# Kernel tuning notes

Hardware: AMD Instinct MI355X
Metric: run time of the kernel (lower is better)

Reference implementation:

```python
import jax, jax.numpy as jnp
import numpy as np

G = 128          # grid_size
C = 256          # feature_dim
H = 4            # n_heads
D = C // H       # d_head
LN_EPS = 1e-5


def setup_inputs() -> dict:
    key = jax.random.key(0)
    ks = jax.random.split(key, 8)
    B, N = 2, 100000
    inp = {
        "GS_feats": jax.random.normal(ks[0], (B, N, C), jnp.float32),
        "scene_bounds": jnp.array([-1.0, 1.0, -1.0, 1.0, -1.0, 1.0], jnp.float32),
        "q_xy": jax.random.normal(ks[1], (C, G, G), jnp.float32),
        "q_xz": jax.random.normal(ks[2], (C, G, G), jnp.float32),
        "q_yz": jax.random.normal(ks[3], (C, G, G), jnp.float32),
        "to_k_w": jax.random.normal(ks[4], (C, C), jnp.float32) * (C ** -0.5),
        "to_k_b": jnp.zeros((C,), jnp.float32),
        "to_v_w": jax.random.normal(ks[5], (C, C), jnp.float32) * (C ** -0.5),
        "to_v_b": jnp.zeros((C,), jnp.float32),
        "ln_g": jnp.ones((C,), jnp.float32),
        "ln_b": jnp.zeros((C,), jnp.float32),
    }
    return inp


def _layernorm(x, g, b):
    mu = jnp.mean(x, axis=-1, keepdims=True)
    var = jnp.mean(jnp.square(x - mu), axis=-1, keepdims=True)
    return (x - mu) * jax.lax.rsqrt(var + LN_EPS) * g + b


def _forward(GS_feats, scene_bounds, q_xy, q_xz, q_yz,
             to_k_w, to_k_b, to_v_w, to_v_b, ln_g, ln_b):
    lo = scene_bounds[0::2]  # (xmin, ymin, zmin)
    hi = scene_bounds[1::2]  # (xmax, ymax, zmax)
    G2 = G * G

    def per_batch(pts):  # pts: [N, C]
        # normalize xyz to [-1, 1] per scene bounds, keep remaining channels
        coords = 2.0 * (pts[:, :3] - lo) / (hi - lo) - 1.0          # [N, 3]
        feats = jnp.concatenate([coords, pts[:, 3:]], axis=-1)      # [N, C]
        fn = _layernorm(feats, ln_g, ln_b)
        k = (fn @ to_k_w.T + to_k_b).reshape(-1, H, D)              # [N, H, D]
        v = (fn @ to_v_w.T + to_v_b).reshape(-1, H, D)              # [N, H, D]

        planes = []
        for q_param, (a0, a1) in ((q_xy, (0, 1)), (q_xz, (0, 2)), (q_yz, (1, 2))):
            pc = coords[:, (a0, a1)]                                 # [N, 2]
            gc = ((pc * 0.5 + 0.5) * (G - 1)).astype(jnp.int32)
            gc = jnp.clip(gc, 0, G - 1)
            idx = gc[:, 0] * G + gc[:, 1]                            # cell per point
            # per-cell learned queries: [G2, H, D]
            qc = q_param.reshape(C, G2).T.reshape(G2, H, D)
            s = jnp.sum(k * qc[idx], axis=-1)                        # [N, H] scores
            # segment softmax over points within each cell
            smax = jax.ops.segment_max(s, idx, num_segments=G2)      # [G2, H]
            smax = jnp.where(jnp.isfinite(smax), smax, 0.0)          # empty cells
            e = jnp.exp(s - smax[idx])                               # [N, H]
            den = jax.ops.segment_sum(e, idx, num_segments=G2)       # [G2, H]
            w = e / jnp.maximum(den[idx], 1e-30)                     # [N, H]
            out = jax.ops.segment_sum(w[:, :, None] * v, idx, num_segments=G2)  # [G2,H,D]
            # original does .view(C, G, G) on the [G2, C] tensor (raw reshape)
            planes.append(out.reshape(G2, C).reshape(C, G, G))
        return jnp.stack(planes)                                     # [3, C, G, G]

    return jax.vmap(per_batch)(GS_feats)                             # [B, 3, C, G, G]


def reference(GS_feats, scene_bounds, q_xy, q_xz, q_yz,
              to_k_w, to_k_b, to_v_w, to_v_b, ln_g, ln_b):
    return _forward(GS_feats, scene_bounds, q_xy, q_xz, q_yz,
                    to_k_w, to_k_b, to_v_w, to_v_b, ln_g, ln_b)
```

## Files before the change

kernel.cpp:

```cpp
#include <hip/hip_runtime.h>
#include <hip/hip_bf16.h>

#define GG 128
#define G2 (GG*GG)
#define CC 256
#define HH 4
#define NPTS 100000
#define NB 2
#define LN_EPS 1e-5f
#define CHUNK 256

typedef __attribute__((ext_vector_type(8))) short short8v;
typedef __attribute__((ext_vector_type(4))) float float4v;

__device__ __forceinline__ unsigned short bfround(float x){
    unsigned u = __float_as_uint(x);
    return (unsigned short)((u + 0x7FFFu + ((u >> 16) & 1u)) >> 16);
}
__device__ __forceinline__ float bfval(unsigned short h){
    return __uint_as_float(((unsigned)h) << 16);
}

__global__ __launch_bounds__(256) void prep_b2_kernel(
    const float* __restrict__ Wk, const float* __restrict__ Wv,
    const float* __restrict__ kb, const float* __restrict__ vb,
    unsigned short* __restrict__ B2, float* __restrict__ bias_comb)
{
    int n = blockIdx.x;
    int t = threadIdx.x;
    const float* src = (n < 256) ? (Wk + (size_t)n*CC) : (Wv + (size_t)(n-256)*CC);
    float w = src[t];
    unsigned short h = bfround(w);
    unsigned short l = bfround(w - bfval(h));
    unsigned short* row = B2 + (size_t)n*768;
    row[t] = h;
    row[256 + t] = l;
    row[512 + t] = h;
    if (t == 0) bias_comb[n] = (n < 256) ? kb[n] : vb[n-256];
}

__global__ __launch_bounds__(256) void transpose_q_kernel(
    const float* __restrict__ qxy, const float* __restrict__ qxz,
    const float* __restrict__ qyz, float* __restrict__ qT)
{
    int blk = blockIdx.x;
    int plane = blk >> 10;
    int rem = blk & 1023;
    int cell0 = (rem >> 2) << 6;
    int c0 = (rem & 3) << 6;
    const float* q = plane == 0 ? qxy : (plane == 1 ? qxz : qyz);
    __shared__ float tile[64][65];
    int tx = threadIdx.x & 63;
    int ty = threadIdx.x >> 6;
    #pragma unroll
    for (int i = ty; i < 64; i += 4)
        tile[i][tx] = q[(size_t)(c0 + i)*G2 + cell0 + tx];
    __syncthreads();
    #pragma unroll
    for (int i = ty; i < 64; i += 4)
        qT[((size_t)plane*G2 + cell0 + i)*CC + c0 + tx] = tile[tx][i];
}

__global__ __launch_bounds__(256, 4) void point_kernel(
    const float* __restrict__ feats, const float* __restrict__ bounds,
    const unsigned short* __restrict__ B2, const float* __restrict__ bias_comb,
    const float* __restrict__ lng, const float* __restrict__ lnb,
    const float* __restrict__ qT,
    unsigned short* __restrict__ Vout, float* __restrict__ s_out,
    int* __restrict__ cnt)
{
    __shared__ __align__(16) char lraw[34176];
    unsigned short* Ahi = (unsigned short*)lraw;
    unsigned short* Alo = (unsigned short*)(lraw + 16896);
    float* K_f = (float*)lraw;
    float* coords_lds = (float*)(lraw + 33792);

    int t = threadIdx.x;
    int lane = t & 63;
    int w = t >> 6;
    long long g0 = (long long)blockIdx.x * 32;
    int b  = (int)(g0 / NPTS);
    int pt0 = (int)(g0 % NPTS);

    float xr[8][4];
    #pragma unroll
    for (int r = 0; r < 8; r++){
        int p = w*8 + r;
        const float* f = feats + ((size_t)b*NPTS + pt0 + p)*CC;
        xr[r][0] = f[lane];
        xr[r][1] = f[lane + 64];
        xr[r][2] = f[lane + 128];
        xr[r][3] = f[lane + 192];
    }

    float lg0 = lng[lane], lg1 = lng[lane+64], lg2 = lng[lane+128], lg3 = lng[lane+192];
    float lb0 = lnb[lane], lb1 = lnb[lane+64], lb2 = lnb[lane+128], lb3 = lnb[lane+192];
    #pragma unroll
    for (int r = 0; r < 8; r++){
        int p = w*8 + r;
        float x0 = xr[r][0], x1 = xr[r][1], x2 = xr[r][2], x3 = xr[r][3];
        if (lane < 3){
            float l0 = bounds[2*lane], h0 = bounds[2*lane+1];
            float tnum = __fmul_rn(2.0f, __fsub_rn(x0, l0));
            float cv = __fsub_rn(__fdiv_rn(tnum, __fsub_rn(h0, l0)), 1.0f);
            x0 = cv;
            coords_lds[p*3 + lane] = cv;
        }
        float s1 = x0 + x1 + x2 + x3;
        float s2 = x0*x0 + x1*x1 + x2*x2 + x3*x3;
        #pragma unroll
        for (int off = 32; off; off >>= 1){
            s1 += __shfl_xor(s1, off);
            s2 += __shfl_xor(s2, off);
        }
        float mu = s1 * (1.0f/CC);
        float var = s2 * (1.0f/CC) - mu*mu;
        float rs = rsqrtf(var + LN_EPS);

        float f0 = (x0 - mu)*rs*lg0 + lb0;
        float f1 = (x1 - mu)*rs*lg1 + lb1;
        float f2 = (x2 - mu)*rs*lg2 + lb2;
        float f3 = (x3 - mu)*rs*lg3 + lb3;
        unsigned short h0 = bfround(f0), h1 = bfround(f1);
        unsigned short h2 = bfround(f2), h3 = bfround(f3);
        Ahi[p*264 + lane      ] = h0;  Alo[p*264 + lane      ] = bfround(f0 - bfval(h0));
        Ahi[p*264 + lane +  64] = h1;  Alo[p*264 + lane +  64] = bfround(f1 - bfval(h1));
        Ahi[p*264 + lane + 128] = h2;  Alo[p*264 + lane + 128] = bfround(f2 - bfval(h2));
        Ahi[p*264 + lane + 192] = h3;  Alo[p*264 + lane + 192] = bfround(f3 - bfval(h3));
    }
    __syncthreads();

    {
        int apt = lane & 15;
        int krow = (lane >> 4) * 8;
        int n0 = w * 128;
        int bcol = n0 + (lane & 15);
        float4v acc0[8], acc1[8];
        #pragma unroll
        for (int ni = 0; ni < 8; ni++){
            float bz = bias_comb[n0 + ni*16 + (lane & 15)];
            acc0[ni][0]=bz; acc0[ni][1]=bz; acc0[ni][2]=bz; acc0[ni][3]=bz;
            acc1[ni][0]=bz; acc1[ni][1]=bz; acc1[ni][2]=bz; acc1[ni][3]=bz;
        }
        #pragma unroll 2
        for (int ks = 0; ks < 24; ks++){
            int term = ks >> 3;
            int kk = (ks & 7)*32 + krow;
            int kglob = term*256 + kk;
            const unsigned short* Abase = (term < 2) ? Ahi : Alo;
            short8v a0 = *reinterpret_cast<const short8v*>(Abase + apt*264 + kk);
            short8v a1 = *reinterpret_cast<const short8v*>(Abase + (16+apt)*264 + kk);
            #pragma unroll
            for (int ni = 0; ni < 8; ni++){
                short8v bf = *reinterpret_cast<const short8v*>(
                    B2 + (size_t)(bcol + ni*16)*768 + kglob);
                acc0[ni] = __builtin_amdgcn_mfma_f32_16x16x32_bf16(a0, bf, acc0[ni], 0, 0, 0);
                acc1[ni] = __builtin_amdgcn_mfma_f32_16x16x32_bf16(a1, bf, acc1[ni], 0, 0, 0);
            }
        }
        __syncthreads();
        if (w < 2){
            #pragma unroll
            for (int ni = 0; ni < 8; ni++){
                int ch = n0 + ni*16 + (lane & 15);
                #pragma unroll
                for (int r4 = 0; r4 < 4; r4++){
                    int pt = (lane >> 4)*4 + r4;
                    K_f[pt*260 + ch]        = acc0[ni][r4];
                    K_f[(16 + pt)*260 + ch] = acc1[ni][r4];
                }
            }
        } else {
            #pragma unroll
            for (int ni = 0; ni < 8; ni++){
                int ch = (n0 - 256) + ni*16 + (lane & 15);
                #pragma unroll
                for (int r4 = 0; r4 < 4; r4++){
                    int pt = (lane >> 4)*4 + r4;
                    Vout[((size_t)b*NPTS + pt0 + pt)*CC + ch]        = bfround(acc0[ni][r4]);
                    Vout[((size_t)b*NPTS + pt0 + 16 + pt)*CC + ch]   = bfround(acc1[ni][r4]);
                }
            }
        }
    }
    __syncthreads();

    {
        int grp = lane >> 3;
        int g   = lane & 7;
        int h   = g >> 1;
        int p   = w*8 + grp;
        int pt  = pt0 + p;
        float cx = coords_lds[p*3], cy = coords_lds[p*3+1], cz = coords_lds[p*3+2];

        float4 k4[8];
        {
            const float4* Krow = reinterpret_cast<const float4*>(&K_f[p*260 + g*32]);
            #pragma unroll
            for (int j = 0; j < 8; j++) k4[j] = Krow[j];
        }
        int cells[3];
        #pragma unroll
        for (int pl = 0; pl < 3; pl++){
            float a = (pl == 2) ? cy : cx;
            float bb = (pl == 0) ? cy : cz;
            float ua = __fmul_rn(__fadd_rn(__fmul_rn(a, 0.5f), 0.5f), (float)(GG-1));
            float ub = __fmul_rn(__fadd_rn(__fmul_rn(bb,0.5f), 0.5f), (float)(GG-1));
            int gx = (int)ua; gx = gx < 0 ? 0 : (gx > GG-1 ? GG-1 : gx);
            int gy = (int)ub; gy = gy < 0 ? 0 : (gy > GG-1 ? GG-1 : gy);
            cells[pl] = gx*GG + gy;
        }
        #pragma unroll
        for (int pl = 0; pl < 3; pl++){
            int cell = cells[pl];
            const float4* qrow = reinterpret_cast<const float4*>(
                qT + ((size_t)pl*G2 + cell)*CC + g*32);
            float a0 = 0.f, a1 = 0.f, a2 = 0.f, a3 = 0.f;
            #pragma unroll
            for (int j = 0; j < 8; j++){
                float4 q4 = qrow[j];
                a0 = fmaf(k4[j].x, q4.x, a0);
                a1 = fmaf(k4[j].y, q4.y, a1);
                a2 = fmaf(k4[j].z, q4.z, a2);
                a3 = fmaf(k4[j].w, q4.w, a3);
            }
            float sh = (a0 + a1) + (a2 + a3);
            sh += __shfl_xor(sh, 1);
            if ((lane & 1) == 0){
                int bp = b*3 + pl;
                s_out[((size_t)bp*NPTS + pt)*HH + h] = sh;
                if (g == 0) atomicAdd(&cnt[(size_t)bp*G2 + cell], 1);
            }
        }
    }
}

__global__ __launch_bounds__(1024) void scan_kernel(
    const int* __restrict__ cnt, int* __restrict__ startm,
    int* __restrict__ worklist, int* __restrict__ nwork)
{
    __shared__ int sums[1024];
    __shared__ int sumc[1024];
    const int PER = (NB*3*G2) / 1024;
    int t = threadIdx.x;
    int base = t * PER;
    int s = 0, sc = 0;
    for (int i = 0; i < PER; i++){
        int c = cnt[base + i];
        s += c;
        sc += (c + CHUNK-1) >> 8;
    }
    sums[t] = s; sumc[t] = sc;
    __syncthreads();
    for (int off = 1; off < 1024; off <<= 1){
        int v  = (t >= off) ? sums[t - off] : 0;
        int vc = (t >= off) ? sumc[t - off] : 0;
        __syncthreads();
        sums[t] += v; sumc[t] += vc;
        __syncthreads();
    }
    int excl  = (t == 0) ? 0 : sums[t - 1];
    int exclc = (t == 0) ? 0 : sumc[t - 1];
    for (int i = 0; i < PER; i++){
        int c = cnt[base + i];
        startm[base + i] = excl;
        excl += c;
        int nch = (c + CHUNK-1) >> 8;
        for (int ci = 0; ci < nch; ci++)
            worklist[exclc++] = ((base + i) << 8) | ci;
    }
    if (t == 1023) nwork[0] = exclc;
}

__global__ __launch_bounds__(256) void fill_kernel(
    const float* __restrict__ feats, const float* __restrict__ bounds,
    int* __restrict__ startm, int* __restrict__ plist)
{
    int g = blockIdx.x * 256 + threadIdx.x;
    if (g >= NB*NPTS) return;
    int b = g / NPTS, pt = g % NPTS;
    const float* f = feats + (size_t)g*CC;
    float c3[3];
    #pragma unroll
    for (int a = 0; a < 3; a++){
        float lo = bounds[2*a], hi = bounds[2*a+1];
        float tn = __fmul_rn(2.0f, __fsub_rn(f[a], lo));
        c3[a] = __fsub_rn(__fdiv_rn(tn, __fsub_rn(hi, lo)), 1.0f);
    }
    #pragma unroll
    for (int pl = 0; pl < 3; pl++){
        float a = (pl == 2) ? c3[1] : c3[0];
        float bb = (pl == 0) ? c3[1] : c3[2];
        float ua = __fmul_rn(__fadd_rn(__fmul_rn(a, 0.5f), 0.5f), (float)(GG-1));
        float ub = __fmul_rn(__fadd_rn(__fmul_rn(bb,0.5f), 0.5f), (float)(GG-1));
        int gx = (int)ua; gx = gx < 0 ? 0 : (gx > GG-1 ? GG-1 : gx);
        int gy = (int)ub; gy = gy < 0 ? 0 : (gy > GG-1 ? GG-1 : gy);
        int cellg = (b*3 + pl)*G2 + gx*GG + gy;
        int pos = atomicAdd(&startm[cellg], 1);
        plist[pos] = pt;
    }
}

__global__ __launch_bounds__(256) void gather_kernel(
    const int* __restrict__ plist, const int* __restrict__ startm,
    const int* __restrict__ cnt, const float* __restrict__ s_in,
    const unsigned short* __restrict__ V, const int* __restrict__ worklist,
    const int* __restrict__ nwork, float* __restrict__ out,
    float* __restrict__ den_tmp)
{
    int lane = threadIdx.x & 63;
    int wi = blockIdx.x * 4 + (threadIdx.x >> 6);
    if (wi >= nwork[0]) return;
    int item = worklist[wi];
    int cellg = item >> 8;
    int ci = item & 255;
    int bp = cellg >> 14;
    int b = bp / 3;
    int h = lane >> 4;

    int end = startm[cellg];
    int n = cnt[cellg];
    int begin = end - n;

    const unsigned short* Vb = V + (size_t)b*NPTS*CC;
    const float* sb = s_in + (size_t)bp*NPTS*HH;

    float m0 = -INFINITY, m1 = -INFINITY, m2 = -INFINITY, m3 = -INFINITY;
    for (int chunk = begin; chunk < end; chunk += 64){
        int i = chunk + lane;
        if (i < end){
            int p = plist[i];
            float4 sv = *reinterpret_cast<const float4*>(sb + (size_t)p*HH);
            m0 = fmaxf(m0, sv.x); m1 = fmaxf(m1, sv.y);
            m2 = fmaxf(m2, sv.z); m3 = fmaxf(m3, sv.w);
        }
    }
    #pragma unroll
    for (int off = 32; off; off >>= 1){
        m0 = fmaxf(m0, __shfl_xor(m0, off));
        m1 = fmaxf(m1, __shfl_xor(m1, off));
        m2 = fmaxf(m2, __shfl_xor(m2, off));
        m3 = fmaxf(m3, __shfl_xor(m3, off));
    }
    float smh = (h == 0) ? m0 : (h == 1) ? m1 : (h == 2) ? m2 : m3;

    int cb = begin + ci*CHUNK;
    int ce = min(cb + CHUNK, end);
    float ax = 0.f, ay = 0.f, az = 0.f, aw = 0.f, den = 0.f;
    for (int chunk = cb; chunk < ce; chunk += 64){
        int m = min(64, ce - chunk);
        int pid = (lane < m) ? plist[chunk + lane] : 0;
        int j = 0;
        for (; j + 4 <= m; j += 4){
            int p0 = __shfl(pid, j  ), p1 = __shfl(pid, j+1);
            int p2 = __shfl(pid, j+2), p3 = __shfl(pid, j+3);
            float e0 = expf(sb[(size_t)p0*HH + h] - smh);
            float e1 = expf(sb[(size_t)p1*HH + h] - smh);
            float e2 = expf(sb[(size_t)p2*HH + h] - smh);
            float e3 = expf(sb[(size_t)p3*HH + h] - smh);
            ushort4 v0 = reinterpret_cast<const ushort4*>(Vb + (size_t)p0*CC)[lane];
            ushort4 v1 = reinterpret_cast<const ushort4*>(Vb + (size_t)p1*CC)[lane];
            ushort4 v2 = reinterpret_cast<const ushort4*>(Vb + (size_t)p2*CC)[lane];
            ushort4 v3 = reinterpret_cast<const ushort4*>(Vb + (size_t)p3*CC)[lane];
            ax = fmaf(e0, bfval(v0.x), ax); ay = fmaf(e0, bfval(v0.y), ay);
            az = fmaf(e0, bfval(v0.z), az); aw = fmaf(e0, bfval(v0.w), aw);
            ax = fmaf(e1, bfval(v1.x), ax); ay = fmaf(e1, bfval(v1.y), ay);
            az = fmaf(e1, bfval(v1.z), az); aw = fmaf(e1, bfval(v1.w), aw);
            ax = fmaf(e2, bfval(v2.x), ax); ay = fmaf(e2, bfval(v2.y), ay);
            az = fmaf(e2, bfval(v2.z), az); aw = fmaf(e2, bfval(v2.w), aw);
            ax = fmaf(e3, bfval(v3.x), ax); ay = fmaf(e3, bfval(v3.y), ay);
            az = fmaf(e3, bfval(v3.z), az); aw = fmaf(e3, bfval(v3.w), aw);
            den += (e0 + e1) + (e2 + e3);
        }
        for (; j < m; ++j){
            int p0 = __shfl(pid, j);
            float e0 = expf(sb[(size_t)p0*HH + h] - smh);
            ushort4 v0 = reinterpret_cast<const ushort4*>(Vb + (size_t)p0*CC)[lane];
            ax = fmaf(e0, bfval(v0.x), ax); ay = fmaf(e0, bfval(v0.y), ay);
            az = fmaf(e0, bfval(v0.z), az); aw = fmaf(e0, bfval(v0.w), aw);
            den += e0;
        }
    }

    if (n <= CHUNK){
        float d = fmaxf(den, 1e-30f);
        float4 o = make_float4(ax/d, ay/d, az/d, aw/d);
        reinterpret_cast<float4*>(out + (size_t)cellg*CC)[lane] = o;
    } else {
        float* op = out + (size_t)cellg*CC + lane*4;
        atomicAdd(&op[0], ax);
        atomicAdd(&op[1], ay);
        atomicAdd(&op[2], az);
        atomicAdd(&op[3], aw);
        if ((lane & 15) == 0)
            atomicAdd(&den_tmp[(size_t)cellg*HH + h], den);
    }
}

__global__ __launch_bounds__(256) void final_norm_kernel(
    const int* __restrict__ cnt, const float* __restrict__ den_tmp,
    float* __restrict__ out)
{
    int t = threadIdx.x;
    int lane = t & 63;
    int cellg = blockIdx.x * 4 + (t >> 6);
    if (cnt[cellg] <= CHUNK) return;
    float d = fmaxf(den_tmp[(size_t)cellg*HH + (lane >> 4)], 1e-30f);
    float4* o4 = reinterpret_cast<float4*>(out + (size_t)cellg*CC);
    float4 v = o4[lane];
    v.x /= d; v.y /= d; v.z /= d; v.w /= d;
    o4[lane] = v;
}

extern "C" void kernel_launch(void* const* d_in, const int* in_sizes, int n_in,
                              void* d_out, int out_size, void* d_ws, size_t ws_size,
                              hipStream_t stream)
{
    const float* feats  = (const float*)d_in[0];
    const float* bounds = (const float*)d_in[1];
    const float* qxy = (const float*)d_in[2];
    const float* qxz = (const float*)d_in[3];
    const float* qyz = (const float*)d_in[4];
    const float* Wk  = (const float*)d_in[5];
    const float* kb  = (const float*)d_in[6];
    const float* Wv  = (const float*)d_in[7];
    const float* vb  = (const float*)d_in[8];
    const float* lng = (const float*)d_in[9];
    const float* lnb = (const float*)d_in[10];

    char* ws = (char*)d_ws;
    float* qT            = (float*)(ws);
    unsigned short* B2   = (unsigned short*)(ws + 50331648);
    float* bias_comb     = (float*)(ws + 51118080);
    unsigned short* Vbuf = (unsigned short*)(ws + 51120128);
    float* s_buf         = (float*)(ws + 153520128);
    int* cnt             = (int*)(ws + 163120128);
    int* startm          = (int*)(ws + 163513344);
    int* plist           = (int*)(ws + 163906560);
    int* worklist        = (int*)(ws + 166306560);
    float* den_tmp       = (float*)(ws + 166748928);
    int* nwork           = (int*)(ws + 168321792);
    if (ws_size < 168321796ull) return;

    hipMemsetAsync(d_out, 0, (size_t)out_size * sizeof(float), stream);
    hipMemsetAsync(den_tmp, 0, (size_t)NB*3*G2*HH*sizeof(float), stream);
    hipMemsetAsync(cnt, 0, (size_t)NB*3*G2*sizeof(int), stream);
    prep_b2_kernel<<<512, 256, 0, stream>>>(Wk, Wv, kb, vb, B2, bias_comb);
    transpose_q_kernel<<<3072, 256, 0, stream>>>(qxy, qxz, qyz, qT);
    point_kernel<<<6250, 256, 0, stream>>>(feats, bounds, B2, bias_comb,
                                           lng, lnb, qT, Vbuf, s_buf, cnt);
    scan_kernel<<<1, 1024, 0, stream>>>(cnt, startm, worklist, nwork);
    fill_kernel<<<(NB*NPTS + 255)/256, 256, 0, stream>>>(feats, bounds, startm, plist);
    gather_kernel<<<27648, 256, 0, stream>>>(plist, startm, cnt, s_buf,
                                             Vbuf, worklist, nwork,
                                             (float*)d_out, den_tmp);
    final_norm_kernel<<<24576, 256, 0, stream>>>(cnt, den_tmp, (float*)d_out);
}
```

Measured before the change: 1.217 ms.

## Split point kernel into GEMM and score kernels, cache cell indices

Splits the fused point kernel into a GEMM kernel that writes K to global memory plus cell indices and counts, and a separate score kernel that reads K and the per-cell queries. The fill kernel reuses the stored cell indices instead of rereading the features. The GEMM kernel drops the LDS round-trip for K and unrolls the k-loop further, aiming for better occupancy and overlap of the scattered q gathers. In exchange it writes and rereads roughly 200 MB of fp32 K through HBM. This path runs only when the workspace is large enough; otherwise the old fused path is kept.

```diff
diff --git a/kernel.cpp b/kernel.cpp
--- a/kernel.cpp
+++ b/kernel.cpp
@@ -61,18 +61,16 @@
         qT[((size_t)plane*G2 + cell0 + i)*CC + c0 + tx] = tile[tx][i];
 }
 
-__global__ __launch_bounds__(256, 4) void point_kernel(
+__global__ __launch_bounds__(256, 4) void gemm_kernel(
     const float* __restrict__ feats, const float* __restrict__ bounds,
     const unsigned short* __restrict__ B2, const float* __restrict__ bias_comb,
     const float* __restrict__ lng, const float* __restrict__ lnb,
-    const float* __restrict__ qT,
-    unsigned short* __restrict__ Vout, float* __restrict__ s_out,
-    int* __restrict__ cnt)
+    unsigned short* __restrict__ Vout, float* __restrict__ Kout,
+    int* __restrict__ cells, int* __restrict__ cnt)
 {
     __shared__ __align__(16) char lraw[34176];
     unsigned short* Ahi = (unsigned short*)lraw;
     unsigned short* Alo = (unsigned short*)(lraw + 16896);
-    float* K_f = (float*)lraw;
     float* coords_lds = (float*)(lraw + 33792);
 
     int t = threadIdx.x;
@@ -130,6 +128,210 @@
     }
     __syncthreads();
 
+    if (lane < 24){
+        int r = lane / 3;
+        int pl = lane - 3*r;
+        int p = w*8 + r;
+        int pt = pt0 + p;
+        float cx = coords_lds[p*3], cy = coords_lds[p*3+1], cz = coords_lds[p*3+2];
+        float a = (pl == 2) ? cy : cx;
+        float bb = (pl == 0) ? cy : cz;
+        float ua = __fmul_rn(__fadd_rn(__fmul_rn(a, 0.5f), 0.5f), (float)(GG-1));
+        float ub = __fmul_rn(__fadd_rn(__fmul_rn(bb,0.5f), 0.5f), (float)(GG-1));
+        int gx = (int)ua; gx = gx < 0 ? 0 : (gx > GG-1 ? GG-1 : gx);
+        int gy = (int)ub; gy = gy < 0 ? 0 : (gy > GG-1 ? GG-1 : gy);
+        int cell = gx*GG + gy;
+        int bp = b*3 + pl;
+        cells[(size_t)bp*NPTS + pt] = cell;
+        atomicAdd(&cnt[(size_t)bp*G2 + cell], 1);
+    }
+
+    {
+        int apt = lane & 15;
+        int krow = (lane >> 4) * 8;
+        int n0 = w * 128;
+        int bcol = n0 + (lane & 15);
+        float4v acc0[8], acc1[8];
+        #pragma unroll
+        for (int ni = 0; ni < 8; ni++){
+            float bz = bias_comb[n0 + ni*16 + (lane & 15)];
+            acc0[ni][0]=bz; acc0[ni][1]=bz; acc0[ni][2]=bz; acc0[ni][3]=bz;
+            acc1[ni][0]=bz; acc1[ni][1]=bz; acc1[ni][2]=bz; acc1[ni][3]=bz;
+        }
+        #pragma unroll 4
+        for (int ks = 0; ks < 24; ks++){
+            int term = ks >> 3;
+            int kk = (ks & 7)*32 + krow;
+            int kglob = term*256 + kk;
+            const unsigned short* Abase = (term < 2) ? Ahi : Alo;
+            short8v a0 = *reinterpret_cast<const short8v*>(Abase + apt*264 + kk);
+            short8v a1 = *reinterpret_cast<const short8v*>(Abase + (16+apt)*264 + kk);
+            #pragma unroll
+            for (int ni = 0; ni < 8; ni++){
+                short8v bf = *reinterpret_cast<const short8v*>(
+                    B2 + (size_t)(bcol + ni*16)*768 + kglob);
+                acc0[ni] = __builtin_amdgcn_mfma_f32_16x16x32_bf16(a0, bf, acc0[ni], 0, 0, 0);
+                acc1[ni] = __builtin_amdgcn_mfma_f32_16x16x32_bf16(a1, bf, acc1[ni], 0, 0, 0);
+            }
+        }
+        if (w < 2){
+            #pragma unroll
+            for (int ni = 0; ni < 8; ni++){
+                int ch = n0 + ni*16 + (lane & 15);
+                #pragma unroll
+                for (int r4 = 0; r4 < 4; r4++){
+                    int pt = (lane >> 4)*4 + r4;
+                    Kout[(size_t)(g0 + pt)*CC + ch]      = acc0[ni][r4];
+                    Kout[(size_t)(g0 + 16 + pt)*CC + ch] = acc1[ni][r4];
+                }
+            }
+        } else {
+            #pragma unroll
+            for (int ni = 0; ni < 8; ni++){
+                int ch = (n0 - 256) + ni*16 + (lane & 15);
+                #pragma unroll
+                for (int r4 = 0; r4 < 4; r4++){
+                    int pt = (lane >> 4)*4 + r4;
+                    Vout[(size_t)(g0 + pt)*CC + ch]      = bfround(acc0[ni][r4]);
+                    Vout[(size_t)(g0 + 16 + pt)*CC + ch] = bfround(acc1[ni][r4]);
+                }
+            }
+        }
+    }
+}
+
+__global__ __launch_bounds__(256) void s_kernel(
+    const float* __restrict__ Kin, const float* __restrict__ qT,
+    const int* __restrict__ cells, float* __restrict__ s_out)
+{
+    int t = threadIdx.x;
+    int lane = t & 63;
+    int w = t >> 6;
+    long long g0 = (long long)blockIdx.x * 32;
+    int b  = (int)(g0 / NPTS);
+    int pt0 = (int)(g0 % NPTS);
+
+    int grp = lane >> 3;
+    int g   = lane & 7;
+    int h   = g >> 1;
+    int p   = w*8 + grp;
+    int pt  = pt0 + p;
+    long long gpt = g0 + p;
+
+    float4 k4[8];
+    {
+        const float4* Krow = reinterpret_cast<const float4*>(
+            Kin + (size_t)gpt*CC + g*32);
+        #pragma unroll
+        for (int j = 0; j < 8; j++) k4[j] = Krow[j];
+    }
+    int c3[3];
+    #pragma unroll
+    for (int pl = 0; pl < 3; pl++)
+        c3[pl] = cells[(size_t)(b*3 + pl)*NPTS + pt];
+
+    #pragma unroll
+    for (int pl = 0; pl < 3; pl++){
+        const float4* qrow = reinterpret_cast<const float4*>(
+            qT + ((size_t)pl*G2 + c3[pl])*CC + g*32);
+        float a0 = 0.f, a1 = 0.f, a2 = 0.f, a3 = 0.f;
+        #pragma unroll
+        for (int j = 0; j < 8; j++){
+            float4 q4 = qrow[j];
+            a0 = fmaf(k4[j].x, q4.x, a0);
+            a1 = fmaf(k4[j].y, q4.y, a1);
+            a2 = fmaf(k4[j].z, q4.z, a2);
+            a3 = fmaf(k4[j].w, q4.w, a3);
+        }
+        float sh = (a0 + a1) + (a2 + a3);
+        sh += __shfl_xor(sh, 1);
+        if ((lane & 1) == 0)
+            s_out[((size_t)(b*3 + pl)*NPTS + pt)*HH + h] = sh;
+    }
+}
+
+__global__ __launch_bounds__(256) void fill_kernel(
+    const int* __restrict__ cells, int* __restrict__ startm,
+    int* __restrict__ plist)
+{
+    int g = blockIdx.x * 256 + threadIdx.x;
+    if (g >= NB*NPTS) return;
+    int b = g / NPTS, pt = g % NPTS;
+    #pragma unroll
+    for (int pl = 0; pl < 3; pl++){
+        int bp = b*3 + pl;
+        int cell = cells[(size_t)bp*NPTS + pt];
+        int pos = atomicAdd(&startm[(size_t)bp*G2 + cell], 1);
+        plist[pos] = pt;
+    }
+}
+
+__global__ __launch_bounds__(256, 4) void point_fused_kernel(
+    const float* __restrict__ feats, const float* __restrict__ bounds,
+    const unsigned short* __restrict__ B2, const float* __restrict__ bias_comb,
+    const float* __restrict__ lng, const float* __restrict__ lnb,
+    const float* __restrict__ qT,
+    unsigned short* __restrict__ Vout, float* __restrict__ s_out,
+    int* __restrict__ cnt)
+{
+    __shared__ __align__(16) char lraw[34176];
+    unsigned short* Ahi = (unsigned short*)lraw;
+    unsigned short* Alo = (unsigned short*)(lraw + 16896);
+    float* K_f = (float*)lraw;
+    float* coords_lds = (float*)(lraw + 33792);
+
+    int t = threadIdx.x;
+    int lane = t & 63;
+    int w = t >> 6;
+    long long g0 = (long long)blockIdx.x * 32;
+    int b  = (int)(g0 / NPTS);
+    int pt0 = (int)(g0 % NPTS);
+
+    float xr[8][4];
+    #pragma unroll
+    for (int r = 0; r < 8; r++){
+        int p = w*8 + r;
+        const float* f = feats + ((size_t)b*NPTS + pt0 + p)*CC;
+        xr[r][0] = f[lane];
+        xr[r][1] = f[lane + 64];
+        xr[r][2] = f[lane + 128];
+        xr[r][3] = f[lane + 192];
+    }
+    float lg0 = lng[lane], lg1 = lng[lane+64], lg2 = lng[lane+128], lg3 = lng[lane+192];
+    float lb0 = lnb[lane], lb1 = lnb[lane+64], lb2 = lnb[lane+128], lb3 = lnb[lane+192];
+    #pragma unroll
+    for (int r = 0; r < 8; r++){
+        int p = w*8 + r;
+        float x0 = xr[r][0], x1 = xr[r][1], x2 = xr[r][2], x3 = xr[r][3];
+        if (lane < 3){
+            float l0 = bounds[2*lane], h0 = bounds[2*lane+1];
+            float tnum = __fmul_rn(2.0f, __fsub_rn(x0, l0));
+            float cv = __fsub_rn(__fdiv_rn(tnum, __fsub_rn(h0, l0)), 1.0f);
+            x0 = cv;
+            coords_lds[p*3 + lane] = cv;
+        }
+        float s1 = x0 + x1 + x2 + x3;
+        float s2 = x0*x0 + x1*x1 + x2*x2 + x3*x3;
+        #pragma unroll
+        for (int off = 32; off; off >>= 1){
+            s1 += __shfl_xor(s1, off);
+            s2 += __shfl_xor(s2, off);
+        }
+        float mu = s1 * (1.0f/CC);
+        float var = s2 * (1.0f/CC) - mu*mu;
+        float rs = rsqrtf(var + LN_EPS);
+        float f0 = (x0 - mu)*rs*lg0 + lb0;
+        float f1 = (x1 - mu)*rs*lg1 + lb1;
+        float f2 = (x2 - mu)*rs*lg2 + lb2;
+        float f3 = (x3 - mu)*rs*lg3 + lb3;
+        unsigned short h0 = bfround(f0), h1 = bfround(f1);
+        unsigned short h2 = bfround(f2), h3 = bfround(f3);
+        Ahi[p*264 + lane      ] = h0;  Alo[p*264 + lane      ] = bfround(f0 - bfval(h0));
+        Ahi[p*264 + lane +  64] = h1;  Alo[p*264 + lane +  64] = bfround(f1 - bfval(h1));
+        Ahi[p*264 + lane + 128] = h2;  Alo[p*264 + lane + 128] = bfround(f2 - bfval(h2));
+        Ahi[p*264 + lane + 192] = h3;  Alo[p*264 + lane + 192] = bfround(f3 - bfval(h3));
+    }
+    __syncthreads();
     {
         int apt = lane & 15;
         int krow = (lane >> 4) * 8;
@@ -177,14 +379,13 @@
                 #pragma unroll
                 for (int r4 = 0; r4 < 4; r4++){
                     int pt = (lane >> 4)*4 + r4;
-                    Vout[((size_t)b*NPTS + pt0 + pt)*CC + ch]        = bfround(acc0[ni][r4]);
-                    Vout[((size_t)b*NPTS + pt0 + 16 + pt)*CC + ch]   = bfround(acc1[ni][r4]);
+                    Vout[((size_t)b*NPTS + pt0 + pt)*CC + ch]      = bfround(acc0[ni][r4]);
+                    Vout[((size_t)b*NPTS + pt0 + 16 + pt)*CC + ch] = bfround(acc1[ni][r4]);
                 }
             }
         }
     }
     __syncthreads();
-
     {
         int grp = lane >> 3;
         int g   = lane & 7;
@@ -192,14 +393,13 @@
         int p   = w*8 + grp;
         int pt  = pt0 + p;
         float cx = coords_lds[p*3], cy = coords_lds[p*3+1], cz = coords_lds[p*3+2];
-
         float4 k4[8];
         {
             const float4* Krow = reinterpret_cast<const float4*>(&K_f[p*260 + g*32]);
             #pragma unroll
             for (int j = 0; j < 8; j++) k4[j] = Krow[j];
         }
-        int cells[3];
+        int cells_[3];
         #pragma unroll
         for (int pl = 0; pl < 3; pl++){
             float a = (pl == 2) ? cy : cx;
@@ -208,11 +408,11 @@
             float ub = __fmul_rn(__fadd_rn(__fmul_rn(bb,0.5f), 0.5f), (float)(GG-1));
             int gx = (int)ua; gx = gx < 0 ? 0 : (gx > GG-1 ? GG-1 : gx);
             int gy = (int)ub; gy = gy < 0 ? 0 : (gy > GG-1 ? GG-1 : gy);
-            cells[pl] = gx*GG + gy;
+            cells_[pl] = gx*GG + gy;
         }
         #pragma unroll
         for (int pl = 0; pl < 3; pl++){
-            int cell = cells[pl];
+            int cell = cells_[pl];
             const float4* qrow = reinterpret_cast<const float4*>(
                 qT + ((size_t)pl*G2 + cell)*CC + g*32);
             float a0 = 0.f, a1 = 0.f, a2 = 0.f, a3 = 0.f;
@@ -232,6 +432,35 @@
                 if (g == 0) atomicAdd(&cnt[(size_t)bp*G2 + cell], 1);
             }
         }
+    }
+}
+
+__global__ __launch_bounds__(256) void fill_feats_kernel(
+    const float* __restrict__ feats, const float* __restrict__ bounds,
+    int* __restrict__ startm, int* __restrict__ plist)
+{
+    int g = blockIdx.x * 256 + threadIdx.x;
+    if (g >= NB*NPTS) return;
+    int b = g / NPTS, pt = g % NPTS;
+    const float* f = feats + (size_t)g*CC;
+    float c3[3];
+    #pragma unroll
+    for (int a = 0; a < 3; a++){
+        float lo = bounds[2*a], hi = bounds[2*a+1];
+        float tn = __fmul_rn(2.0f, __fsub_rn(f[a], lo));
+        c3[a] = __fsub_rn(__fdiv_rn(tn, __fsub_rn(hi, lo)), 1.0f);
+    }
+    #pragma unroll
+    for (int pl = 0; pl < 3; pl++){
+        float a = (pl == 2) ? c3[1] : c3[0];
+        float bb = (pl == 0) ? c3[1] : c3[2];
+        float ua = __fmul_rn(__fadd_rn(__fmul_rn(a, 0.5f), 0.5f), (float)(GG-1));
+        float ub = __fmul_rn(__fadd_rn(__fmul_rn(bb,0.5f), 0.5f), (float)(GG-1));
+        int gx = (int)ua; gx = gx < 0 ? 0 : (gx > GG-1 ? GG-1 : gx);
+        int gy = (int)ub; gy = gy < 0 ? 0 : (gy > GG-1 ? GG-1 : gy);
+        int cellg = (b*3 + pl)*G2 + gx*GG + gy;
+        int pos = atomicAdd(&startm[cellg], 1);
+        plist[pos] = pt;
     }
 }
 
@@ -270,35 +499,6 @@
             worklist[exclc++] = ((base + i) << 8) | ci;
     }
     if (t == 1023) nwork[0] = exclc;
-}
-
-__global__ __launch_bounds__(256) void fill_kernel(
-    const float* __restrict__ feats, const float* __restrict__ bounds,
-    int* __restrict__ startm, int* __restrict__ plist)
-{
-    int g = blockIdx.x * 256 + threadIdx.x;
-    if (g >= NB*NPTS) return;
-    int b = g / NPTS, pt = g % NPTS;
-    const float* f = feats + (size_t)g*CC;
-    float c3[3];
-    #pragma unroll
-    for (int a = 0; a < 3; a++){
-        float lo = bounds[2*a], hi = bounds[2*a+1];
-        float tn = __fmul_rn(2.0f, __fsub_rn(f[a], lo));
-        c3[a] = __fsub_rn(__fdiv_rn(tn, __fsub_rn(hi, lo)), 1.0f);
-    }
-    #pragma unroll
-    for (int pl = 0; pl < 3; pl++){
-        float a = (pl == 2) ? c3[1] : c3[0];
-        float bb = (pl == 0) ? c3[1] : c3[2];
-        float ua = __fmul_rn(__fadd_rn(__fmul_rn(a, 0.5f), 0.5f), (float)(GG-1));
-        float ub = __fmul_rn(__fadd_rn(__fmul_rn(bb,0.5f), 0.5f), (float)(GG-1));
-        int gx = (int)ua; gx = gx < 0 ? 0 : (gx > GG-1 ? GG-1 : gx);
-        int gy = (int)ub; gy = gy < 0 ? 0 : (gy > GG-1 ? GG-1 : gy);
-        int cellg = (b*3 + pl)*G2 + gx*GG + gy;
-        int pos = atomicAdd(&startm[cellg], 1);
-        plist[pos] = pt;
-    }
 }
 
 __global__ __launch_bounds__(256) void gather_kernel(
@@ -440,17 +640,32 @@
     int* worklist        = (int*)(ws + 166306560);
     float* den_tmp       = (float*)(ws + 166748928);
     int* nwork           = (int*)(ws + 168321792);
-    if (ws_size < 168321796ull) return;
+    int* cells           = (int*)(ws + 168321920);
+    float* Kbuf          = (float*)(ws + 170721920);
+    const size_t NEED_SPLIT = 375521920ull;
+    const size_t NEED_FUSED = 168321920ull;
+
+    if (ws_size < NEED_FUSED) return;
 
     hipMemsetAsync(d_out, 0, (size_t)out_size * sizeof(float), stream);
     hipMemsetAsync(den_tmp, 0, (size_t)NB*3*G2*HH*sizeof(float), stream);
     hipMemsetAsync(cnt, 0, (size_t)NB*3*G2*sizeof(int), stream);
     prep_b2_kernel<<<512, 256, 0, stream>>>(Wk, Wv, kb, vb, B2, bias_comb);
     transpose_q_kernel<<<3072, 256, 0, stream>>>(qxy, qxz, qyz, qT);
-    point_kernel<<<6250, 256, 0, stream>>>(feats, bounds, B2, bias_comb,
-                                           lng, lnb, qT, Vbuf, s_buf, cnt);
-    scan_kernel<<<1, 1024, 0, stream>>>(cnt, startm, worklist, nwork);
-    fill_kernel<<<(NB*NPTS + 255)/256, 256, 0, stream>>>(feats, bounds, startm, plist);
+
+    if (ws_size >= NEED_SPLIT){
+        gemm_kernel<<<6250, 256, 0, stream>>>(feats, bounds, B2, bias_comb,
+                                              lng, lnb, Vbuf, Kbuf, cells, cnt);
+        s_kernel<<<6250, 256, 0, stream>>>(Kbuf, qT, cells, s_buf);
+        scan_kernel<<<1, 1024, 0, stream>>>(cnt, startm, worklist, nwork);
+        fill_kernel<<<(NB*NPTS + 255)/256, 256, 0, stream>>>(cells, startm, plist);
+    } else {
+        point_fused_kernel<<<6250, 256, 0, stream>>>(feats, bounds, B2, bias_comb,
+                                                     lng, lnb, qT, Vbuf, s_buf, cnt);
+        scan_kernel<<<1, 1024, 0, stream>>>(cnt, startm, worklist, nwork);
+        fill_feats_kernel<<<(NB*NPTS + 255)/256, 256, 0, stream>>>(feats, bounds,
+                                                                   startm, plist);
+    }
     gather_kernel<<<27648, 256, 0, stream>>>(plist, startm, cnt, s_buf,
                                              Vbuf, worklist, nwork,
                                              (float*)d_out, den_tmp);
```

Result: slower. 1.356 ms (+11.4%).

## Process 64 points per block with 4x4 MFMA tiles and cache cell indices

Applied to the files above, without the earlier changes.

The point kernel now handles 64 points per 512-thread block, with each wave computing a 4x4 grid of 16x16 MFMA tiles. Each B2 weight fragment fetched from global memory is reused across four A row-tiles instead of two, which halves weight traffic per point. Cell indices are computed once in the point kernel and stored to a buffer, so the fill kernel reads them instead of re-reading feats and recomputing coordinates. The costs are double the LDS per block, which lowers occupancy, a larger accumulator register footprint, and an extra global buffer of cell indices.

```diff
diff --git a/kernel.cpp b/kernel.cpp
--- a/kernel.cpp
+++ b/kernel.cpp
@@ -61,32 +61,30 @@
         qT[((size_t)plane*G2 + cell0 + i)*CC + c0 + tx] = tile[tx][i];
 }
 
-__global__ __launch_bounds__(256, 4) void point_kernel(
+__global__ __launch_bounds__(512, 4) void point64_kernel(
     const float* __restrict__ feats, const float* __restrict__ bounds,
     const unsigned short* __restrict__ B2, const float* __restrict__ bias_comb,
     const float* __restrict__ lng, const float* __restrict__ lnb,
     const float* __restrict__ qT,
     unsigned short* __restrict__ Vout, float* __restrict__ s_out,
-    int* __restrict__ cnt)
-{
-    __shared__ __align__(16) char lraw[34176];
+    int* __restrict__ cells, int* __restrict__ cnt)
+{
+    __shared__ __align__(16) char lraw[68352];
     unsigned short* Ahi = (unsigned short*)lraw;
-    unsigned short* Alo = (unsigned short*)(lraw + 16896);
+    unsigned short* Alo = (unsigned short*)(lraw + 33792);
     float* K_f = (float*)lraw;
-    float* coords_lds = (float*)(lraw + 33792);
+    float* coords_lds = (float*)(lraw + 67584);
 
     int t = threadIdx.x;
     int lane = t & 63;
     int w = t >> 6;
-    long long g0 = (long long)blockIdx.x * 32;
-    int b  = (int)(g0 / NPTS);
-    int pt0 = (int)(g0 % NPTS);
+    long long g0 = (long long)blockIdx.x * 64;
 
     float xr[8][4];
     #pragma unroll
     for (int r = 0; r < 8; r++){
-        int p = w*8 + r;
-        const float* f = feats + ((size_t)b*NPTS + pt0 + p)*CC;
+        long long gpt = g0 + w*8 + r;
+        const float* f = feats + (size_t)gpt*CC;
         xr[r][0] = f[lane];
         xr[r][1] = f[lane + 64];
         xr[r][2] = f[lane + 128];
@@ -130,17 +128,40 @@
     }
     __syncthreads();
 
+    if (lane < 24){
+        int r = lane / 3;
+        int pl = lane - 3*r;
+        int p = w*8 + r;
+        long long gpt = g0 + p;
+        int bb = (int)(gpt / NPTS);
+        int ptp = (int)(gpt - (long long)bb*NPTS);
+        float cx = coords_lds[p*3], cy = coords_lds[p*3+1], cz = coords_lds[p*3+2];
+        float a = (pl == 2) ? cy : cx;
+        float b2 = (pl == 0) ? cy : cz;
+        float ua = __fmul_rn(__fadd_rn(__fmul_rn(a, 0.5f), 0.5f), (float)(GG-1));
+        float ub = __fmul_rn(__fadd_rn(__fmul_rn(b2,0.5f), 0.5f), (float)(GG-1));
+        int gx = (int)ua; gx = gx < 0 ? 0 : (gx > GG-1 ? GG-1 : gx);
+        int gy = (int)ub; gy = gy < 0 ? 0 : (gy > GG-1 ? GG-1 : gy);
+        int cell = gx*GG + gy;
+        int bp = bb*3 + pl;
+        cells[(size_t)bp*NPTS + ptp] = cell;
+        atomicAdd(&cnt[(size_t)bp*G2 + cell], 1);
+    }
+
     {
         int apt = lane & 15;
         int krow = (lane >> 4) * 8;
-        int n0 = w * 128;
+        int n0 = w * 64;
         int bcol = n0 + (lane & 15);
-        float4v acc0[8], acc1[8];
+        float4v acc[4][4];
         #pragma unroll
-        for (int ni = 0; ni < 8; ni++){
+        for (int ni = 0; ni < 4; ni++){
             float bz = bias_comb[n0 + ni*16 + (lane & 15)];
-            acc0[ni][0]=bz; acc0[ni][1]=bz; acc0[ni][2]=bz; acc0[ni][3]=bz;
-            acc1[ni][0]=bz; acc1[ni][1]=bz; acc1[ni][2]=bz; acc1[ni][3]=bz;
+            #pragma unroll
+            for (int mi = 0; mi < 4; mi++){
+                acc[mi][ni][0]=bz; acc[mi][ni][1]=bz;
+                acc[mi][ni][2]=bz; acc[mi][ni][3]=bz;
+            }
         }
         #pragma unroll 2
         for (int ks = 0; ks < 24; ks++){
@@ -148,38 +169,46 @@
             int kk = (ks & 7)*32 + krow;
             int kglob = term*256 + kk;
             const unsigned short* Abase = (term < 2) ? Ahi : Alo;
-            short8v a0 = *reinterpret_cast<const short8v*>(Abase + apt*264 + kk);
-            short8v a1 = *reinterpret_cast<const short8v*>(Abase + (16+apt)*264 + kk);
-            #pragma unroll
-            for (int ni = 0; ni < 8; ni++){
-                short8v bf = *reinterpret_cast<const short8v*>(
+            short8v a[4];
+            #pragma unroll
+            for (int mi = 0; mi < 4; mi++)
+                a[mi] = *reinterpret_cast<const short8v*>(Abase + (mi*16 + apt)*264 + kk);
+            short8v bf[4];
+            #pragma unroll
+            for (int ni = 0; ni < 4; ni++)
+                bf[ni] = *reinterpret_cast<const short8v*>(
                     B2 + (size_t)(bcol + ni*16)*768 + kglob);
-                acc0[ni] = __builtin_amdgcn_mfma_f32_16x16x32_bf16(a0, bf, acc0[ni], 0, 0, 0);
-                acc1[ni] = __builtin_amdgcn_mfma_f32_16x16x32_bf16(a1, bf, acc1[ni], 0, 0, 0);
-            }
+            #pragma unroll
+            for (int mi = 0; mi < 4; mi++)
+                #pragma unroll
+                for (int ni = 0; ni < 4; ni++)
+                    acc[mi][ni] = __builtin_amdgcn_mfma_f32_16x16x32_bf16(
+                        a[mi], bf[ni], acc[mi][ni], 0, 0, 0);
         }
         __syncthreads();
-        if (w < 2){
-            #pragma unroll
-            for (int ni = 0; ni < 8; ni++){
+        if (w < 4){
+            #pragma unroll
+            for (int ni = 0; ni < 4; ni++){
                 int ch = n0 + ni*16 + (lane & 15);
                 #pragma unroll
-                for (int r4 = 0; r4 < 4; r4++){
-                    int pt = (lane >> 4)*4 + r4;
-                    K_f[pt*260 + ch]        = acc0[ni][r4];
-                    K_f[(16 + pt)*260 + ch] = acc1[ni][r4];
-                }
+                for (int mi = 0; mi < 4; mi++)
+                    #pragma unroll
+                    for (int r4 = 0; r4 < 4; r4++){
+                        int pt = mi*16 + (lane >> 4)*4 + r4;
+                        K_f[pt*260 + ch] = acc[mi][ni][r4];
+                    }
             }
         } else {
             #pragma unroll
-            for (int ni = 0; ni < 8; ni++){
+            for (int ni = 0; ni < 4; ni++){
                 int ch = (n0 - 256) + ni*16 + (lane & 15);
                 #pragma unroll
-                for (int r4 = 0; r4 < 4; r4++){
-                    int pt = (lane >> 4)*4 + r4;
-                    Vout[((size_t)b*NPTS + pt0 + pt)*CC + ch]        = bfround(acc0[ni][r4]);
-                    Vout[((size_t)b*NPTS + pt0 + 16 + pt)*CC + ch]   = bfround(acc1[ni][r4]);
-                }
+                for (int mi = 0; mi < 4; mi++)
+                    #pragma unroll
+                    for (int r4 = 0; r4 < 4; r4++){
+                        int pt = mi*16 + (lane >> 4)*4 + r4;
+                        Vout[(size_t)(g0 + pt)*CC + ch] = bfround(acc[mi][ni][r4]);
+                    }
             }
         }
     }
@@ -190,7 +219,9 @@
         int g   = lane & 7;
         int h   = g >> 1;
         int p   = w*8 + grp;
-        int pt  = pt0 + p;
+        long long gpt = g0 + p;
+        int b  = (int)(gpt / NPTS);
+        int pt = (int)(gpt - (long long)b*NPTS);
         float cx = coords_lds[p*3], cy = coords_lds[p*3+1], cz = coords_lds[p*3+2];
 
         float4 k4[8];
@@ -199,7 +230,7 @@
             #pragma unroll
             for (int j = 0; j < 8; j++) k4[j] = Krow[j];
         }
-        int cells[3];
+        int cells_[3];
         #pragma unroll
         for (int pl = 0; pl < 3; pl++){
             float a = (pl == 2) ? cy : cx;
@@ -208,13 +239,12 @@
             float ub = __fmul_rn(__fadd_rn(__fmul_rn(bb,0.5f), 0.5f), (float)(GG-1));
             int gx = (int)ua; gx = gx < 0 ? 0 : (gx > GG-1 ? GG-1 : gx);
             int gy = (int)ub; gy = gy < 0 ? 0 : (gy > GG-1 ? GG-1 : gy);
-            cells[pl] = gx*GG + gy;
+            cells_[pl] = gx*GG + gy;
         }
         #pragma unroll
         for (int pl = 0; pl < 3; pl++){
-            int cell = cells[pl];
             const float4* qrow = reinterpret_cast<const float4*>(
-                qT + ((size_t)pl*G2 + cell)*CC + g*32);
+                qT + ((size_t)pl*G2 + cells_[pl])*CC + g*32);
             float a0 = 0.f, a1 = 0.f, a2 = 0.f, a3 = 0.f;
             #pragma unroll
             for (int j = 0; j < 8; j++){
@@ -226,12 +256,25 @@
             }
             float sh = (a0 + a1) + (a2 + a3);
             sh += __shfl_xor(sh, 1);
-            if ((lane & 1) == 0){
-                int bp = b*3 + pl;
-                s_out[((size_t)bp*NPTS + pt)*HH + h] = sh;
-                if (g == 0) atomicAdd(&cnt[(size_t)bp*G2 + cell], 1);
-            }
-        }
+            if ((lane & 1) == 0)
+                s_out[((size_t)(b*3 + pl)*NPTS + pt)*HH + h] = sh;
+        }
+    }
+}
+
+__global__ __launch_bounds__(256) void fill_kernel(
+    const int* __restrict__ cells, int* __restrict__ startm,
+    int* __restrict__ plist)
+{
+    int g = blockIdx.x * 256 + threadIdx.x;
+    if (g >= NB*NPTS) return;
+    int b = g / NPTS, pt = g % NPTS;
+    #pragma unroll
+    for (int pl = 0; pl < 3; pl++){
+        int bp = b*3 + pl;
+        int cell = cells[(size_t)bp*NPTS + pt];
+        int pos = atomicAdd(&startm[(size_t)bp*G2 + cell], 1);
+        plist[pos] = pt;
     }
 }
 
@@ -270,35 +313,6 @@
             worklist[exclc++] = ((base + i) << 8) | ci;
     }
     if (t == 1023) nwork[0] = exclc;
-}
-
-__global__ __launch_bounds__(256) void fill_kernel(
-    const float* __restrict__ feats, const float* __restrict__ bounds,
-    int* __restrict__ startm, int* __restrict__ plist)
-{
-    int g = blockIdx.x * 256 + threadIdx.x;
-    if (g >= NB*NPTS) return;
-    int b = g / NPTS, pt = g % NPTS;
-    const float* f = feats + (size_t)g*CC;
-    float c3[3];
-    #pragma unroll
-    for (int a = 0; a < 3; a++){
-        float lo = bounds[2*a], hi = bounds[2*a+1];
-        float tn = __fmul_rn(2.0f, __fsub_rn(f[a], lo));
-        c3[a] = __fsub_rn(__fdiv_rn(tn, __fsub_rn(hi, lo)), 1.0f);
-    }
-    #pragma unroll
-    for (int pl = 0; pl < 3; pl++){
-        float a = (pl == 2) ? c3[1] : c3[0];
-        float bb = (pl == 0) ? c3[1] : c3[2];
-        float ua = __fmul_rn(__fadd_rn(__fmul_rn(a, 0.5f), 0.5f), (float)(GG-1));
-        float ub = __fmul_rn(__fadd_rn(__fmul_rn(bb,0.5f), 0.5f), (float)(GG-1));
-        int gx = (int)ua; gx = gx < 0 ? 0 : (gx > GG-1 ? GG-1 : gx);
-        int gy = (int)ub; gy = gy < 0 ? 0 : (gy > GG-1 ? GG-1 : gy);
-        int cellg = (b*3 + pl)*G2 + gx*GG + gy;
-        int pos = atomicAdd(&startm[cellg], 1);
-        plist[pos] = pt;
-    }
 }
 
 __global__ __launch_bounds__(256) void gather_kernel(
@@ -440,17 +454,19 @@
     int* worklist        = (int*)(ws + 166306560);
     float* den_tmp       = (float*)(ws + 166748928);
     int* nwork           = (int*)(ws + 168321792);
-    if (ws_size < 168321796ull) return;
+    int* cells           = (int*)(ws + 168321920);
+    if (ws_size < 170721920ull) return;
 
     hipMemsetAsync(d_out, 0, (size_t)out_size * sizeof(float), stream);
     hipMemsetAsync(den_tmp, 0, (size_t)NB*3*G2*HH*sizeof(float), stream);
     hipMemsetAsync(cnt, 0, (size_t)NB*3*G2*sizeof(int), stream);
     prep_b2_kernel<<<512, 256, 0, stream>>>(Wk, Wv, kb, vb, B2, bias_comb);
     transpose_q_kernel<<<3072, 256, 0, stream>>>(qxy, qxz, qyz, qT);
-    point_kernel<<<6250, 256, 0, stream>>>(feats, bounds, B2, bias_comb,
-                                           lng, lnb, qT, Vbuf, s_buf, cnt);
+    point64_kernel<<<3125, 512, 0, stream>>>(feats, bounds, B2, bias_comb,
+                                             lng, lnb, qT, Vbuf, s_buf,
+                                             cells, cnt);
     scan_kernel<<<1, 1024, 0, stream>>>(cnt, startm, worklist, nwork);
-    fill_kernel<<<(NB*NPTS + 255)/256, 256, 0, stream>>>(feats, bounds, startm, plist);
+    fill_kernel<<<(NB*NPTS + 255)/256, 256, 0, stream>>>(cells, startm, plist);
     gather_kernel<<<27648, 256, 0, stream>>>(plist, startm, cnt, s_buf,
                                              Vbuf, worklist, nwork,
                                              (float*)d_out, den_tmp);
```

After: 981.9 us (median of 2 runs). -19.3%, faster.
